# Kernel tuning notes

Measured on AMD Instinct MI355X. Metric: run time of the kernel, lower is better.

## Reference

```python
import jax, jax.numpy as jnp
import numpy as np
from jax import lax

B, T, C = 4, 2048, 1024
E, DFF, TOPK = 8, 4096, 2


def setup_inputs() -> dict:
    key = jax.random.key(0)
    ks = jax.random.split(key, 5)
    scale = 0.02
    x = jax.random.normal(ks[0], (B, T, C), dtype=jnp.float32)
    router_w = jax.random.normal(ks[1], (C, E), dtype=jnp.float32) * scale
    router_b = jnp.zeros((E,), dtype=jnp.float32)
    w1 = jax.random.normal(ks[2], (E, C, DFF), dtype=jnp.float32) * scale
    b1 = jnp.zeros((E, DFF), dtype=jnp.float32)
    w2 = jax.random.normal(ks[3], (E, DFF, C), dtype=jnp.float32) * scale
    b2 = jnp.zeros((E, C), dtype=jnp.float32)
    return {"x": x, "router_w": router_w, "router_b": router_b,
            "w1": w1, "b1": b1, "w2": w2, "b2": b2, "top_k": TOPK}


def reference(x, router_w, router_b, w1, b1, w2, b2, top_k):
    # Router: softmax then top-k (matches torch.topk(F.softmax(logits)))
    logits = jnp.einsum('btc,ce->bte', x, router_w) + router_b   # [B,T,E]
    probs = jax.nn.softmax(logits, axis=-1)
    weights, indices = lax.top_k(probs, top_k)                    # [B,T,k]
    n_exp = w1.shape[0]
    # Combined per-expert weight per token (sum over top-k slots hitting expert j)
    onehot = jax.nn.one_hot(indices, n_exp, dtype=x.dtype)        # [B,T,k,E]
    cw = jnp.sum(weights[..., None] * onehot, axis=-2)            # [B,T,E]
    bsz, seq, dim = x.shape
    flat_x = x.reshape(-1, dim)                                   # [N,C]
    flat_cw = cw.reshape(-1, n_exp)                               # [N,E]
    out = jnp.zeros_like(flat_x)
    for j in range(n_exp):  # fixed small expert loop (dropout=0 -> eval)
        h = jax.nn.gelu(flat_x @ w1[j] + b1[j], approximate=False)
        out = out + flat_cw[:, j:j + 1] * (h @ w2[j] + b2[j])
    return out.reshape(bsz, seq, dim)
```

## Files before the change

### kernel.cpp

```cpp
#include <hip/hip_runtime.h>
#include <math.h>

typedef __bf16 bf16;
typedef bf16 bf16x4 __attribute__((ext_vector_type(4)));
typedef bf16 bf16x8 __attribute__((ext_vector_type(8)));
typedef float f32x4 __attribute__((ext_vector_type(4)));

#define NTOK 8192
#define CDIM 1024
#define EXP 8
#define DFF 4096
#define BM 256
#define BN 256
#define BK 64

__device__ __forceinline__ void gld_lds16(const bf16* g, bf16* l) {
  __builtin_amdgcn_global_load_lds(
      (const __attribute__((address_space(1))) unsigned int*)g,
      (__attribute__((address_space(3))) unsigned int*)l, 16, 0, 0);
}

__global__ __launch_bounds__(256) void convert_x(const float* __restrict__ in,
                                                 bf16* __restrict__ out) {
  int idx = (blockIdx.x * 256 + threadIdx.x) * 8;
  float4 a = *(const float4*)(in + idx);
  float4 b = *(const float4*)(in + idx + 4);
  bf16x8 v;
  v[0] = (bf16)a.x; v[1] = (bf16)a.y; v[2] = (bf16)a.z; v[3] = (bf16)a.w;
  v[4] = (bf16)b.x; v[5] = (bf16)b.y; v[6] = (bf16)b.z; v[7] = (bf16)b.w;
  *(bf16x8*)(out + idx) = v;
}

__global__ __launch_bounds__(256) void transpose_cvt(
    const float* __restrict__ in, bf16* __restrict__ out, int R, int Cin) {
  __shared__ float tile[32][33];
  int e = blockIdx.z;
  const float* ip = in + (size_t)e * R * Cin;
  bf16* op = out + (size_t)e * R * Cin;
  int c0 = blockIdx.x * 32, r0 = blockIdx.y * 32;
  int tx = threadIdx.x & 31, ty = threadIdx.x >> 5;
#pragma unroll
  for (int i = 0; i < 4; i++)
    tile[ty + 8 * i][tx] = ip[(size_t)(r0 + ty + 8 * i) * Cin + c0 + tx];
  __syncthreads();
  int c = threadIdx.x >> 3, r4 = (threadIdx.x & 7) * 4;
  bf16x4 v;
  v[0] = (bf16)tile[r4][c];
  v[1] = (bf16)tile[r4 + 1][c];
  v[2] = (bf16)tile[r4 + 2][c];
  v[3] = (bf16)tile[r4 + 3][c];
  *(bf16x4*)&op[(size_t)(c0 + c) * R + r0 + r4] = v;
}

__global__ __launch_bounds__(256) void router_kernel(
    const float* __restrict__ x, const float* __restrict__ rw,
    const float* __restrict__ rb, unsigned int* __restrict__ cnt,
    int* __restrict__ list, float* __restrict__ wq) {
  int wave = threadIdx.x >> 6, lane = threadIdx.x & 63;
  int t = blockIdx.x * 4 + wave;
  if (t >= NTOK) return;
  const float* xr = x + (size_t)t * CDIM;
  float acc[8] = {0.f, 0.f, 0.f, 0.f, 0.f, 0.f, 0.f, 0.f};
  for (int c = lane; c < CDIM; c += 64) {
    float xv = xr[c];
    const float4* rp = (const float4*)(rw + c * 8);
    float4 r0 = rp[0], r1 = rp[1];
    acc[0] += xv * r0.x; acc[1] += xv * r0.y;
    acc[2] += xv * r0.z; acc[3] += xv * r0.w;
    acc[4] += xv * r1.x; acc[5] += xv * r1.y;
    acc[6] += xv * r1.z; acc[7] += xv * r1.w;
  }
#pragma unroll
  for (int e = 0; e < 8; e++)
#pragma unroll
    for (int off = 32; off; off >>= 1) acc[e] += __shfl_down(acc[e], off);
  if (lane == 0) {
    float p[8], mx = -1e30f;
#pragma unroll
    for (int e = 0; e < 8; e++) { p[e] = acc[e] + rb[e]; mx = fmaxf(mx, p[e]); }
    float s = 0.f;
#pragma unroll
    for (int e = 0; e < 8; e++) { p[e] = expf(p[e] - mx); s += p[e]; }
    float inv = 1.0f / s;
#pragma unroll
    for (int e = 0; e < 8; e++) p[e] *= inv;
    int i1 = 0;
#pragma unroll
    for (int e = 1; e < 8; e++) if (p[e] > p[i1]) i1 = e;
    int i2 = (i1 == 0) ? 1 : 0;
#pragma unroll
    for (int e = 0; e < 8; e++) if (e != i1 && p[e] > p[i2]) i2 = e;
    unsigned s0 = atomicAdd(&cnt[i1], 1u);
    list[i1 * NTOK + s0] = t * 2;
    unsigned s1 = atomicAdd(&cnt[i2], 1u);
    list[i2 * NTOK + s1] = t * 2 + 1;
    wq[t * 2] = p[i1];
    wq[t * 2 + 1] = p[i2];
  }
}

__global__ __launch_bounds__(512, 2) void gemm1_kernel(
    const bf16* __restrict__ xb, const bf16* __restrict__ w1b,
    const float* __restrict__ b1, const int* __restrict__ list,
    const unsigned int* __restrict__ cnt, bf16* __restrict__ h) {
  int bid = blockIdx.x + 16 * (blockIdx.y + 32 * blockIdx.z);
  int wg = (bid & 7) * 512 + (bid >> 3);
  int n0 = (wg & 15) * BN;
  int mt = (wg >> 4) & 31;
  int e = wg >> 9;
  int count = (int)min(cnt[e], (unsigned)NTOK);
  int m0 = mt * BM;
  if (m0 >= count) return;

  __shared__ __align__(16) bf16 As[BM][BK];
  __shared__ __align__(16) bf16 Bs[BN][BK];

  int tid = threadIdx.x;
  int w = tid >> 6, l = tid & 63;
  int lhi = l >> 3, llo = l & 7;
  int w8l = w * 8 + lhi;
  int dst8 = llo * 8;
  int sc8 = (llo ^ lhi) * 8;

  const int* lp = list + e * NTOK;
  const bf16* aptr[4];
  const bf16* bptr[4];
#pragma unroll
  for (int p = 0; p < 4; p++) {
    int row = p * 64 + w8l;
    int enc = lp[min(m0 + row, count - 1)];
    aptr[p] = xb + (size_t)(enc >> 1) * CDIM + sc8;
    bptr[p] = w1b + (size_t)e * DFF * CDIM + (size_t)(n0 + row) * CDIM + sc8;
  }

  f32x4 acc[8][4] = {};
  int wm = w >> 2, wn = w & 3;
  int ln = l & 15, kq = l >> 4;
  int rx = ln & 7;

  for (int k0 = 0; k0 < CDIM; k0 += BK) {
    __syncthreads();
#pragma unroll
    for (int p = 0; p < 4; p++) {
      gld_lds16(aptr[p] + k0, &As[p * 64 + w8l][dst8]);
      gld_lds16(bptr[p] + k0, &Bs[p * 64 + w8l][dst8]);
    }
    __syncthreads();
#pragma unroll
    for (int hh = 0; hh < 2; hh++) {
      int co = ((hh * 4 + kq) ^ rx) * 8;
      bf16x8 af[8], bfr[4];
#pragma unroll
      for (int j = 0; j < 4; j++)
        bfr[j] = *(bf16x8*)&Bs[wn * 64 + j * 16 + ln][co];
#pragma unroll
      for (int i = 0; i < 8; i++)
        af[i] = *(bf16x8*)&As[wm * 128 + i * 16 + ln][co];
#pragma unroll
      for (int i = 0; i < 8; i++)
#pragma unroll
        for (int j = 0; j < 4; j++)
          acc[i][j] = __builtin_amdgcn_mfma_f32_16x16x32_bf16(
              af[i], bfr[j], acc[i][j], 0, 0, 0);
    }
  }

  float b1f[4];
#pragma unroll
  for (int j = 0; j < 4; j++)
    b1f[j] = b1[e * DFF + n0 + wn * 64 + j * 16 + ln];
#pragma unroll
  for (int i = 0; i < 8; i++) {
#pragma unroll
    for (int r = 0; r < 4; r++) {
      int mrow = wm * 128 + i * 16 + kq * 4 + r;
      if (m0 + mrow < count) {
        int enc = lp[m0 + mrow];
        bf16* hr = h + (size_t)enc * DFF + n0 + wn * 64 + ln;
#pragma unroll
        for (int j = 0; j < 4; j++) {
          float v = acc[i][j][r] + b1f[j];
          float g = 0.5f * v * (1.0f + erff(v * 0.70710678118654752f));
          hr[j * 16] = (bf16)g;
        }
      }
    }
  }
}

__global__ __launch_bounds__(512, 2) void gemm2_kernel(
    const bf16* __restrict__ h, const bf16* __restrict__ w2b,
    const float* __restrict__ b2, const int* __restrict__ list,
    const unsigned int* __restrict__ cnt, const float* __restrict__ wq,
    float* __restrict__ out) {
  int bid = blockIdx.x + 4 * (blockIdx.y + 32 * blockIdx.z);
  int wg = (bid & 7) * 128 + (bid >> 3);
  int n0 = (wg & 3) * BN;
  int mt = (wg >> 2) & 31;
  int e = wg >> 7;
  int count = (int)min(cnt[e], (unsigned)NTOK);
  int m0 = mt * BM;
  if (m0 >= count) return;

  __shared__ __align__(16) bf16 As[BM][BK];
  __shared__ __align__(16) bf16 Bs[BN][BK];

  int tid = threadIdx.x;
  int w = tid >> 6, l = tid & 63;
  int lhi = l >> 3, llo = l & 7;
  int w8l = w * 8 + lhi;
  int dst8 = llo * 8;
  int sc8 = (llo ^ lhi) * 8;

  const int* lp = list + e * NTOK;
  const bf16* aptr[4];
  const bf16* bptr[4];
#pragma unroll
  for (int p = 0; p < 4; p++) {
    int row = p * 64 + w8l;
    int enc = lp[min(m0 + row, count - 1)];
    aptr[p] = h + (size_t)enc * DFF + sc8;
    bptr[p] = w2b + (size_t)e * CDIM * DFF + (size_t)(n0 + row) * DFF + sc8;
  }

  f32x4 acc[8][4] = {};
  int wm = w >> 2, wn = w & 3;
  int ln = l & 15, kq = l >> 4;
  int rx = ln & 7;

  for (int k0 = 0; k0 < DFF; k0 += BK) {
    __syncthreads();
#pragma unroll
    for (int p = 0; p < 4; p++) {
      gld_lds16(aptr[p] + k0, &As[p * 64 + w8l][dst8]);
      gld_lds16(bptr[p] + k0, &Bs[p * 64 + w8l][dst8]);
    }
    __syncthreads();
#pragma unroll
    for (int hh = 0; hh < 2; hh++) {
      int co = ((hh * 4 + kq) ^ rx) * 8;
      bf16x8 af[8], bfr[4];
#pragma unroll
      for (int j = 0; j < 4; j++)
        bfr[j] = *(bf16x8*)&Bs[wn * 64 + j * 16 + ln][co];
#pragma unroll
      for (int i = 0; i < 8; i++)
        af[i] = *(bf16x8*)&As[wm * 128 + i * 16 + ln][co];
#pragma unroll
      for (int i = 0; i < 8; i++)
#pragma unroll
        for (int j = 0; j < 4; j++)
          acc[i][j] = __builtin_amdgcn_mfma_f32_16x16x32_bf16(
              af[i], bfr[j], acc[i][j], 0, 0, 0);
    }
  }

  float b2f[4];
#pragma unroll
  for (int j = 0; j < 4; j++)
    b2f[j] = b2[e * CDIM + n0 + wn * 64 + j * 16 + ln];
#pragma unroll
  for (int i = 0; i < 8; i++) {
#pragma unroll
    for (int r = 0; r < 4; r++) {
      int mrow = wm * 128 + i * 16 + kq * 4 + r;
      if (m0 + mrow < count) {
        int enc = lp[m0 + mrow];
        int t = enc >> 1;
        float wt = wq[enc];
        float* orow = out + (size_t)t * CDIM + n0 + wn * 64 + ln;
#pragma unroll
        for (int j = 0; j < 4; j++)
          atomicAdd(&orow[j * 16], wt * (acc[i][j][r] + b2f[j]));
      }
    }
  }
}

extern "C" void kernel_launch(void* const* d_in, const int* in_sizes, int n_in,
                              void* d_out, int out_size, void* d_ws,
                              size_t ws_size, hipStream_t stream) {
  const float* x = (const float*)d_in[0];
  const float* rw = (const float*)d_in[1];
  const float* rb = (const float*)d_in[2];
  const float* w1 = (const float*)d_in[3];
  const float* b1 = (const float*)d_in[4];
  const float* w2 = (const float*)d_in[5];
  const float* b2 = (const float*)d_in[6];
  float* out = (float*)d_out;

  char* ws = (char*)d_ws;
  size_t o = 0;
  auto carve = [&](size_t bytes) {
    void* p = ws + o;
    o = (o + bytes + 255) & ~(size_t)255;
    return p;
  };
  bf16* w1b = (bf16*)carve((size_t)EXP * DFF * CDIM * 2);
  bf16* w2b = (bf16*)carve((size_t)EXP * DFF * CDIM * 2);
  bf16* h = (bf16*)carve((size_t)2 * NTOK * DFF * 2);
  bf16* xb = (bf16*)carve((size_t)NTOK * CDIM * 2);
  int* list = (int*)carve((size_t)EXP * NTOK * 4);
  float* wq = (float*)carve((size_t)2 * NTOK * 4);
  unsigned int* cnt = (unsigned int*)carve(64);

  hipMemsetAsync(out, 0, (size_t)out_size * sizeof(float), stream);
  hipMemsetAsync(cnt, 0, 64, stream);

  convert_x<<<NTOK * CDIM / (256 * 8), 256, 0, stream>>>(x, xb);
  transpose_cvt<<<dim3(DFF / 32, CDIM / 32, EXP), 256, 0, stream>>>(w1, w1b,
                                                                    CDIM, DFF);
  transpose_cvt<<<dim3(CDIM / 32, DFF / 32, EXP), 256, 0, stream>>>(w2, w2b,
                                                                    DFF, CDIM);
  router_kernel<<<NTOK / 4, 256, 0, stream>>>(x, rw, rb, cnt, list, wq);
  gemm1_kernel<<<dim3(DFF / BN, NTOK / BM, EXP), 512, 0, stream>>>(
      xb, w1b, b1, list, cnt, h);
  gemm2_kernel<<<dim3(CDIM / BN, NTOK / BM, EXP), 512, 0, stream>>>(
      h, w2b, b2, list, cnt, wq, out);
}
```

Before: 1.202 ms.

## Double-buffer LDS in expert GEMMs and replace output atomics with combine pass

Both expert GEMMs now keep two LDS stages. The next K-tile is issued with global-to-LDS loads before the current tile's MFMAs run, and there is one barrier per iteration instead of two. GEMM2 no longer does atomicAdd into the output. It writes weighted per-slot rows into a scratch buffer that reuses the w1 bf16 workspace, and a new elementwise kernel sums the two top-k slots per token. This removes atomic contention and the output memset. The cost is an extra 64MB write plus read, and LDS per block doubles to 128KB, which likely prevents two blocks per CU.

```diff
diff --git a/kernel.cpp b/kernel.cpp
--- a/kernel.cpp
+++ b/kernel.cpp
@@ -112,8 +112,8 @@
   int m0 = mt * BM;
   if (m0 >= count) return;
 
-  __shared__ __align__(16) bf16 As[BM][BK];
-  __shared__ __align__(16) bf16 Bs[BN][BK];
+  __shared__ __align__(16) bf16 As[2][BM][BK];
+  __shared__ __align__(16) bf16 Bs[2][BM][BK];
 
   int tid = threadIdx.x;
   int w = tid >> 6, l = tid & 63;
@@ -138,24 +138,36 @@
   int ln = l & 15, kq = l >> 4;
   int rx = ln & 7;
 
-  for (int k0 = 0; k0 < CDIM; k0 += BK) {
-    __syncthreads();
-#pragma unroll
-    for (int p = 0; p < 4; p++) {
-      gld_lds16(aptr[p] + k0, &As[p * 64 + w8l][dst8]);
-      gld_lds16(bptr[p] + k0, &Bs[p * 64 + w8l][dst8]);
-    }
-    __syncthreads();
+#pragma unroll
+  for (int p = 0; p < 4; p++) {
+    gld_lds16(aptr[p], &As[0][p * 64 + w8l][dst8]);
+    gld_lds16(bptr[p], &Bs[0][p * 64 + w8l][dst8]);
+  }
+  __syncthreads();
+
+  const int NT = CDIM / BK;
+  int cur = 0;
+  for (int t = 0; t < NT; ++t) {
+    if (t + 1 < NT) {
+      int k0 = (t + 1) * BK;
+#pragma unroll
+      for (int p = 0; p < 4; p++) {
+        gld_lds16(aptr[p] + k0, &As[cur ^ 1][p * 64 + w8l][dst8]);
+        gld_lds16(bptr[p] + k0, &Bs[cur ^ 1][p * 64 + w8l][dst8]);
+      }
+    }
+    bf16(*Asc)[BK] = As[cur];
+    bf16(*Bsc)[BK] = Bs[cur];
 #pragma unroll
     for (int hh = 0; hh < 2; hh++) {
       int co = ((hh * 4 + kq) ^ rx) * 8;
       bf16x8 af[8], bfr[4];
 #pragma unroll
       for (int j = 0; j < 4; j++)
-        bfr[j] = *(bf16x8*)&Bs[wn * 64 + j * 16 + ln][co];
+        bfr[j] = *(bf16x8*)&Bsc[wn * 64 + j * 16 + ln][co];
 #pragma unroll
       for (int i = 0; i < 8; i++)
-        af[i] = *(bf16x8*)&As[wm * 128 + i * 16 + ln][co];
+        af[i] = *(bf16x8*)&Asc[wm * 128 + i * 16 + ln][co];
 #pragma unroll
       for (int i = 0; i < 8; i++)
 #pragma unroll
@@ -163,6 +175,8 @@
           acc[i][j] = __builtin_amdgcn_mfma_f32_16x16x32_bf16(
               af[i], bfr[j], acc[i][j], 0, 0, 0);
     }
+    __syncthreads();
+    cur ^= 1;
   }
 
   float b1f[4];
@@ -192,7 +206,7 @@
     const bf16* __restrict__ h, const bf16* __restrict__ w2b,
     const float* __restrict__ b2, const int* __restrict__ list,
     const unsigned int* __restrict__ cnt, const float* __restrict__ wq,
-    float* __restrict__ out) {
+    float* __restrict__ y) {
   int bid = blockIdx.x + 4 * (blockIdx.y + 32 * blockIdx.z);
   int wg = (bid & 7) * 128 + (bid >> 3);
   int n0 = (wg & 3) * BN;
@@ -202,8 +216,8 @@
   int m0 = mt * BM;
   if (m0 >= count) return;
 
-  __shared__ __align__(16) bf16 As[BM][BK];
-  __shared__ __align__(16) bf16 Bs[BN][BK];
+  __shared__ __align__(16) bf16 As[2][BM][BK];
+  __shared__ __align__(16) bf16 Bs[2][BM][BK];
 
   int tid = threadIdx.x;
   int w = tid >> 6, l = tid & 63;
@@ -228,24 +242,36 @@
   int ln = l & 15, kq = l >> 4;
   int rx = ln & 7;
 
-  for (int k0 = 0; k0 < DFF; k0 += BK) {
-    __syncthreads();
-#pragma unroll
-    for (int p = 0; p < 4; p++) {
-      gld_lds16(aptr[p] + k0, &As[p * 64 + w8l][dst8]);
-      gld_lds16(bptr[p] + k0, &Bs[p * 64 + w8l][dst8]);
-    }
-    __syncthreads();
+#pragma unroll
+  for (int p = 0; p < 4; p++) {
+    gld_lds16(aptr[p], &As[0][p * 64 + w8l][dst8]);
+    gld_lds16(bptr[p], &Bs[0][p * 64 + w8l][dst8]);
+  }
+  __syncthreads();
+
+  const int NT = DFF / BK;
+  int cur = 0;
+  for (int t = 0; t < NT; ++t) {
+    if (t + 1 < NT) {
+      int k0 = (t + 1) * BK;
+#pragma unroll
+      for (int p = 0; p < 4; p++) {
+        gld_lds16(aptr[p] + k0, &As[cur ^ 1][p * 64 + w8l][dst8]);
+        gld_lds16(bptr[p] + k0, &Bs[cur ^ 1][p * 64 + w8l][dst8]);
+      }
+    }
+    bf16(*Asc)[BK] = As[cur];
+    bf16(*Bsc)[BK] = Bs[cur];
 #pragma unroll
     for (int hh = 0; hh < 2; hh++) {
       int co = ((hh * 4 + kq) ^ rx) * 8;
       bf16x8 af[8], bfr[4];
 #pragma unroll
       for (int j = 0; j < 4; j++)
-        bfr[j] = *(bf16x8*)&Bs[wn * 64 + j * 16 + ln][co];
+        bfr[j] = *(bf16x8*)&Bsc[wn * 64 + j * 16 + ln][co];
 #pragma unroll
       for (int i = 0; i < 8; i++)
-        af[i] = *(bf16x8*)&As[wm * 128 + i * 16 + ln][co];
+        af[i] = *(bf16x8*)&Asc[wm * 128 + i * 16 + ln][co];
 #pragma unroll
       for (int i = 0; i < 8; i++)
 #pragma unroll
@@ -253,6 +279,8 @@
           acc[i][j] = __builtin_amdgcn_mfma_f32_16x16x32_bf16(
               af[i], bfr[j], acc[i][j], 0, 0, 0);
     }
+    __syncthreads();
+    cur ^= 1;
   }
 
   float b2f[4];
@@ -266,15 +294,27 @@
       int mrow = wm * 128 + i * 16 + kq * 4 + r;
       if (m0 + mrow < count) {
         int enc = lp[m0 + mrow];
-        int t = enc >> 1;
         float wt = wq[enc];
-        float* orow = out + (size_t)t * CDIM + n0 + wn * 64 + ln;
+        float* yr = y + (size_t)enc * CDIM + n0 + wn * 64 + ln;
 #pragma unroll
         for (int j = 0; j < 4; j++)
-          atomicAdd(&orow[j * 16], wt * (acc[i][j][r] + b2f[j]));
+          yr[j * 16] = wt * (acc[i][j][r] + b2f[j]);
       }
     }
   }
+}
+
+__global__ __launch_bounds__(256) void combine_kernel(
+    const float* __restrict__ y, float* __restrict__ out) {
+  int idx = (blockIdx.x * 256 + threadIdx.x) * 4;
+  int t = idx >> 10;
+  int c = idx & 1023;
+  const float* y0 = y + ((size_t)(t * 2) << 10) + c;
+  float4 a = *(const float4*)y0;
+  float4 b = *(const float4*)(y0 + CDIM);
+  float4 r;
+  r.x = a.x + b.x; r.y = a.y + b.y; r.z = a.z + b.z; r.w = a.w + b.w;
+  *(float4*)(out + idx) = r;
 }
 
 extern "C" void kernel_launch(void* const* d_in, const int* in_sizes, int n_in,
@@ -303,8 +343,8 @@
   int* list = (int*)carve((size_t)EXP * NTOK * 4);
   float* wq = (float*)carve((size_t)2 * NTOK * 4);
   unsigned int* cnt = (unsigned int*)carve(64);
-
-  hipMemsetAsync(out, 0, (size_t)out_size * sizeof(float), stream);
+  float* y = (float*)w1b;
+
   hipMemsetAsync(cnt, 0, 64, stream);
 
   convert_x<<<NTOK * CDIM / (256 * 8), 256, 0, stream>>>(x, xb);
@@ -316,5 +356,6 @@
   gemm1_kernel<<<dim3(DFF / BN, NTOK / BM, EXP), 512, 0, stream>>>(
       xb, w1b, b1, list, cnt, h);
   gemm2_kernel<<<dim3(CDIM / BN, NTOK / BM, EXP), 512, 0, stream>>>(
-      h, w2b, b2, list, cnt, wq, out);
-}
+      h, w2b, b2, list, cnt, wq, y);
+  combine_kernel<<<NTOK * CDIM / (256 * 4), 256, 0, stream>>>(y, out);
+}
```

Result: faster. 1.108 ms (-7.8%).
